# Performance work log

Measured on AMD Instinct MI355X. Metric: run time of the kernel, lower is better.

Reference implementation:

```python
import jax, jax.numpy as jnp
import numpy as np

MARGIN = 1.0  # cur_margin for LBA_inverted_loss=True
COS_SCALE = 128.0


def smoothed_metric_loss(X, margin=MARGIN):
    # X: [B, E]. Lifted structured loss with inverted cosine similarity.
    B = X.shape[0]
    P = B // 2
    D = (X @ X.T) / COS_SCALE            # [B, B]
    E = jnp.exp(margin + D)              # [B, B]
    # For pair p (rows i=2p, j=2p+1): sum E over rows {i,j}, all columns except {i,j}.
    Eb = E.reshape(P, 2, P, 2)           # [P, 2, P, 2]
    row_sums = Eb.sum(axis=(1, 2, 3))    # [P] full sum over both rows of pair p
    idx = jnp.arange(P)
    diag_block = Eb[idx, :, idx, :].sum(axis=(1, 2))  # [P] the excluded 2x2 block
    S = row_sums - diag_block            # [P] masked sums
    Dij = D.reshape(P, 2, P, 2)[idx, 0, idx, 1]       # [P] D[i, j]
    J = jnp.log(S) - Dij
    return 0.5 * jnp.mean(J * J)


def reference(text_embeddings, shape_embeddings):
    B = text_embeddings.shape[0]
    # shape_embeddings repeated twice per model: row k -> shape[k // 2]
    shape_rep = jnp.repeat(shape_embeddings, 2, axis=0)      # [B, E]
    metric_tt = smoothed_metric_loss(text_embeddings)
    # mask rows: even rows keep text, odd rows take repeated shape embedding
    even = (jnp.arange(B) % 2 == 0)[:, None]
    mixed = jnp.where(even, text_embeddings, shape_rep)      # [B, E]
    metric_st = smoothed_metric_loss(mixed)
    return metric_tt + metric_st


def setup_inputs() -> dict:
    key = jax.random.key(0)
    k1, k2 = jax.random.split(key)
    B, E = 8192, 128
    text_embeddings = jax.random.normal(k1, (B, E), dtype=jnp.float32)
    shape_embeddings = jax.random.normal(k2, (B // 2, E), dtype=jnp.float32)
    return {"text_embeddings": text_embeddings, "shape_embeddings": shape_embeddings}
```

## Files before the change

### kernel.cpp

```cpp
#include <hip/hip_runtime.h>
#include <hip/hip_bf16.h>


#define B_ROWS 8192
#define E_COLS 128
#define P_PAIRS 4096
#define NSTRIP 128
#define NHS 6

using f32x4 = __attribute__((ext_vector_type(4))) float;
using i32x8 = __attribute__((ext_vector_type(8))) int;

#define BF_SCALE 0.106164482742544f
#define EULER    2.718281828459045f
#define SCALE1   0x7f

__device__ __forceinline__ unsigned pk4_fp8(float a, float b, float c, float d) {
    unsigned v = 0;
    v = __builtin_amdgcn_cvt_pk_fp8_f32(a * BF_SCALE, b * BF_SCALE, v, false);
    v = __builtin_amdgcn_cvt_pk_fp8_f32(c * BF_SCALE, d * BF_SCALE, v, true);
    return v;
}

__device__ __forceinline__ int lds_off(int row, int k0) {
    return (row << 7) + (k0 ^ ((row & 7) << 4));
}

__device__ __forceinline__ i32x8 load_frag32(const char* base, int row, int k32) {
    union { i32x8 v; int4 h[2]; } u;
    u.h[0] = *(const int4*)(base + lds_off(row, k32));
    u.h[1] = *(const int4*)(base + lds_off(row, k32 + 16));
    return u.v;
}

__device__ __forceinline__ void stage8k(const char* gsrc, char* ldst, int tid) {
#pragma unroll
    for (int it = 0; it < 2; ++it) {
        int L   = it * 4096 + tid * 16;
        int row = L >> 7;
        int cb  = L & 127;
        int src = (row << 7) + (cb ^ ((row & 7) << 4));
        __builtin_amdgcn_global_load_lds(
            (const __attribute__((address_space(1))) void*)(gsrc + src),
            (__attribute__((address_space(3))) void*)(ldst + L), 16, 0, 0);
    }
}

__global__ void convert_kernel(const float* __restrict__ text,
                               const float* __restrict__ shape,
                               unsigned* __restrict__ Xt,
                               unsigned* __restrict__ Xm,
                               float* __restrict__ R,
                               float* __restrict__ out) {
    int idx = blockIdx.x * blockDim.x + threadIdx.x;
    if (idx >= B_ROWS * E_COLS / 4) return;
    if (idx < 4096) {
        float4 z; z.x = z.y = z.z = z.w = 0.f;
        ((float4*)R)[idx] = z;
    }
    if (idx == 0) *out = 0.f;
    int e = idx * 4;
    float4 t = *(const float4*)(text + e);
    unsigned tp = pk4_fp8(t.x, t.y, t.z, t.w);
    Xt[idx] = tp;
    int row = e >> 7;
    if (row & 1) {
        int col = e & 127;
        float4 s = *(const float4*)(shape + (row >> 1) * E_COLS + col);
        Xm[idx] = pk4_fp8(s.x, s.y, s.z, s.w);
    } else {
        Xm[idx] = tp;
    }
}

__launch_bounds__(256, 6)
__global__ void gemm_rowsum_kernel(const unsigned char* __restrict__ Xt,
                                   const unsigned char* __restrict__ Xm,
                                   float* __restrict__ R) {
    const int bm = blockIdx.x, h = blockIdx.y, l = blockIdx.z;
    const char* gX = (const char*)(l ? Xm : Xt);

    __shared__ __align__(16) char buf0[64 * 128];
    __shared__ __align__(16) char buf1[64 * 128];
    const int tid = threadIdx.x;

    const int t0 = h + 1;
    int N = (h < 3) ? 11 : 10;
    const bool do64 = (h == 4 && bm < 64);
    if (do64) N = 11;

    auto tf = [&](int i) -> int { return (h == 4 && i == 10) ? 64 : (t0 + 6 * i); };

    stage8k(gX + (size_t)bm * 8192, buf0, tid);
    stage8k(gX + (size_t)((bm + tf(0)) & 127) * 8192, buf1, tid);
    asm volatile("s_waitcnt vmcnt(2)" ::: "memory");
    __builtin_amdgcn_s_barrier();

    const int lane = tid & 63;
    const int w  = tid >> 6;
    const int wr = w >> 1, wc = w & 1;
    const int rA0 = wr * 32 + (lane & 15);
    const int rB0 = wc * 32 + (lane & 15);
    const int k32 = (lane >> 4) * 32;

    i32x8 afr[2];
#pragma unroll
    for (int m = 0; m < 2; ++m)
        afr[m] = load_frag32(buf0, rA0 + m * 16, k32);

    float s_r[2][4] = {{0.f}};

    if (h == 3) {
        i32x8 bfr[2];
#pragma unroll
        for (int n = 0; n < 2; ++n)
            bfr[n] = load_frag32(buf0, rB0 + n * 16, k32);
        f32x4 acc[2][2] = {};
#pragma unroll
        for (int m = 0; m < 2; ++m)
#pragma unroll
            for (int n = 0; n < 2; ++n)
                acc[m][n] = __builtin_amdgcn_mfma_scale_f32_16x16x128_f8f6f4(
                    afr[m], bfr[n], acc[m][n], 0, 0, 0, SCALE1, 0, SCALE1);
#pragma unroll
        for (int m = 0; m < 2; ++m)
#pragma unroll
            for (int n = 0; n < 2; ++n)
#pragma unroll
                for (int j = 0; j < 4; ++j)
                    s_r[m][j] += __builtin_amdgcn_exp2f(acc[m][n][j]);
    }

    asm volatile("s_waitcnt lgkmcnt(0)" ::: "memory");
    __builtin_amdgcn_s_barrier();

    int cur = 1;
    for (int idx = 0; idx < N; ++idx) {
        const bool hasnext = (idx + 1 < N);
        if (hasnext)
            stage8k(gX + (size_t)((bm + tf(idx + 1)) & 127) * 8192,
                    cur ? buf0 : buf1, tid);

        if (hasnext) { asm volatile("s_waitcnt vmcnt(2)" ::: "memory"); }
        else         { asm volatile("s_waitcnt vmcnt(0)" ::: "memory"); }
        __builtin_amdgcn_s_barrier();

        const char* lsrc = cur ? buf1 : buf0;
        i32x8 bfr[2];
#pragma unroll
        for (int n = 0; n < 2; ++n)
            bfr[n] = load_frag32(lsrc, rB0 + n * 16, k32);
        f32x4 acc[2][2] = {};
#pragma unroll
        for (int m = 0; m < 2; ++m)
#pragma unroll
            for (int n = 0; n < 2; ++n)
                acc[m][n] = __builtin_amdgcn_mfma_scale_f32_16x16x128_f8f6f4(
                    afr[m], bfr[n], acc[m][n], 0, 0, 0, SCALE1, 0, SCALE1);

        asm volatile("s_waitcnt lgkmcnt(0)" ::: "memory");
        __builtin_amdgcn_s_barrier();

        const int bn = (bm + tf(idx)) & 127;
        float s_c[2] = {0.f, 0.f};
#pragma unroll
        for (int m = 0; m < 2; ++m)
#pragma unroll
            for (int n = 0; n < 2; ++n)
#pragma unroll
                for (int j = 0; j < 4; ++j) {
                    float e2 = __builtin_amdgcn_exp2f(acc[m][n][j]);
                    s_r[m][j] += e2;
                    s_c[n] += e2;
                }
#pragma unroll
        for (int n = 0; n < 2; ++n) {
            float v = s_c[n];
            v += __shfl_xor(v, 16, 64);
            v += __shfl_xor(v, 32, 64);
            if (lane < 16) {
                int gcol = bn * 64 + wc * 32 + n * 16 + lane;
                atomicAdd(&R[l * B_ROWS + gcol], EULER * v);
            }
        }
        cur ^= 1;
    }

#pragma unroll
    for (int m = 0; m < 2; ++m)
#pragma unroll
        for (int j = 0; j < 4; ++j) {
            float v = s_r[m][j];
            v += __shfl_xor(v, 1, 64);
            v += __shfl_xor(v, 2, 64);
            v += __shfl_xor(v, 4, 64);
            v += __shfl_xor(v, 8, 64);
            if ((lane & 15) == 0) {
                int grow = bm * 64 + wr * 32 + m * 16 + (lane >> 4) * 4 + j;
                atomicAdd(&R[l * B_ROWS + grow], EULER * v);
            }
        }
}

__global__ void finalize_kernel(const float* __restrict__ text,
                                const float* __restrict__ shape,
                                const float* __restrict__ R,
                                float* __restrict__ out) {
    const int tid = threadIdx.x;
    const int lane = tid & 63;
    const int w = tid >> 6;
    const float inv128 = 0.0078125f;
    float accum = 0.f;

    for (int task = blockIdx.x * 4 + w; task < 2 * P_PAIRS; task += 1024) {
        int l = task >> 12;
        int p = task & (P_PAIRS - 1);
        const float* a = text + (2 * p) * E_COLS;
        const float* b = l ? (shape + p * E_COLS) : (text + (2 * p + 1) * E_COLS);
        float2 av = *(const float2*)(a + lane * 2);
        float2 bv = *(const float2*)(b + lane * 2);
        float dii = av.x * av.x + av.y * av.y;
        float djj = bv.x * bv.x + bv.y * bv.y;
        float dij = av.x * bv.x + av.y * bv.y;
#pragma unroll
        for (int sh = 1; sh < 64; sh <<= 1) {
            dii += __shfl_xor(dii, sh, 64);
            djj += __shfl_xor(djj, sh, 64);
            dij += __shfl_xor(dij, sh, 64);
        }
        if (lane == 0) {
            float Dii = dii * inv128, Djj = djj * inv128, Dij = dij * inv128;
            float S = R[l * B_ROWS + 2 * p] + R[l * B_ROWS + 2 * p + 1]
                    - (__expf(1.f + Dii) + 2.f * __expf(1.f + Dij) + __expf(1.f + Djj));
            float J = __logf(S) - Dij;
            accum += 0.5f * J * J * (1.0f / (float)P_PAIRS);
        }
    }

    __shared__ float red[4];
    if (lane == 0) red[w] = accum;
    __syncthreads();
    if (tid == 0) atomicAdd(out, red[0] + red[1] + red[2] + red[3]);
}

extern "C" void kernel_launch(void* const* d_in, const int* in_sizes, int n_in,
                              void* d_out, int out_size, void* d_ws, size_t ws_size,
                              hipStream_t stream) {
    const float* text  = (const float*)d_in[0];
    const float* shape = (const float*)d_in[1];
    float* out = (float*)d_out;
    char* ws = (char*)d_ws;

    unsigned char* Xt = (unsigned char*)ws;
    unsigned char* Xm = (unsigned char*)(ws + 1u * 1024u * 1024u);
    float* R = (float*)(ws + 2u * 1024u * 1024u);

    convert_kernel<<<(B_ROWS * E_COLS / 4 + 255) / 256, 256, 0, stream>>>(
        text, shape, (unsigned*)Xt, (unsigned*)Xm, R, out);

    dim3 grid(NSTRIP, NHS, 2);
    gemm_rowsum_kernel<<<grid, 256, 0, stream>>>(Xt, Xm, R);

    finalize_kernel<<<256, 256, 0, stream>>>(text, shape, R, out);
}
```

Before: 40.54 us.

## Remap waves to 64x16 column strips with full A-fragment residency

Each wave now holds all four A row fragments and loads a single B fragment per tile, covering a 64x16 strip instead of a 32x32 quadrant. This halves the per-tile B LDS fragment loads and column shuffle/atomic work per wave, and moves the exp2 and accumulation inside the MFMA loop with s_setprio around the MFMAs to interleave with other waves. In exchange each wave keeps more A-fragment and row-sum registers, which may pressure occupancy at launch bounds 256x6, and row-sum atomics at the end double per wave.

After: 72.62 us. 1.79x slower.

```diff
diff --git a/kernel.cpp b/kernel.cpp
--- a/kernel.cpp
+++ b/kernel.cpp
@@ -86,8 +86,7 @@
 
     const int t0 = h + 1;
     int N = (h < 3) ? 11 : 10;
-    const bool do64 = (h == 4 && bm < 64);
-    if (do64) N = 11;
+    if (h == 4 && bm < 64) N = 11;
 
     auto tf = [&](int i) -> int { return (h == 4 && i == 10) ? 64 : (t0 + 6 * i); };
 
@@ -97,38 +96,33 @@
     __builtin_amdgcn_s_barrier();
 
     const int lane = tid & 63;
-    const int w  = tid >> 6;
-    const int wr = w >> 1, wc = w & 1;
-    const int rA0 = wr * 32 + (lane & 15);
-    const int rB0 = wc * 32 + (lane & 15);
-    const int k32 = (lane >> 4) * 32;
-
-    i32x8 afr[2];
-#pragma unroll
-    for (int m = 0; m < 2; ++m)
+    const int w    = tid >> 6;
+    const int rB0  = w * 16 + (lane & 15);
+    const int rA0  = lane & 15;
+    const int k32  = (lane >> 4) * 32;
+
+    i32x8 afr[4];
+#pragma unroll
+    for (int m = 0; m < 4; ++m)
         afr[m] = load_frag32(buf0, rA0 + m * 16, k32);
 
-    float s_r[2][4] = {{0.f}};
+    float s_r[4][4] = {{0.f}};
 
     if (h == 3) {
-        i32x8 bfr[2];
-#pragma unroll
-        for (int n = 0; n < 2; ++n)
-            bfr[n] = load_frag32(buf0, rB0 + n * 16, k32);
-        f32x4 acc[2][2] = {};
-#pragma unroll
-        for (int m = 0; m < 2; ++m)
-#pragma unroll
-            for (int n = 0; n < 2; ++n)
-                acc[m][n] = __builtin_amdgcn_mfma_scale_f32_16x16x128_f8f6f4(
-                    afr[m], bfr[n], acc[m][n], 0, 0, 0, SCALE1, 0, SCALE1);
-#pragma unroll
-        for (int m = 0; m < 2; ++m)
-#pragma unroll
-            for (int n = 0; n < 2; ++n)
-#pragma unroll
-                for (int j = 0; j < 4; ++j)
-                    s_r[m][j] += __builtin_amdgcn_exp2f(acc[m][n][j]);
+        i32x8 dbf = load_frag32(buf0, rB0, k32);
+#pragma unroll
+        for (int mh = 0; mh < 2; ++mh) {
+            f32x4 a0 = {}, a1 = {};
+            a0 = __builtin_amdgcn_mfma_scale_f32_16x16x128_f8f6f4(
+                afr[2 * mh + 0], dbf, a0, 0, 0, 0, SCALE1, 0, SCALE1);
+            a1 = __builtin_amdgcn_mfma_scale_f32_16x16x128_f8f6f4(
+                afr[2 * mh + 1], dbf, a1, 0, 0, 0, SCALE1, 0, SCALE1);
+#pragma unroll
+            for (int j = 0; j < 4; ++j) {
+                s_r[2 * mh + 0][j] += __builtin_amdgcn_exp2f(a0[j]);
+                s_r[2 * mh + 1][j] += __builtin_amdgcn_exp2f(a1[j]);
+            }
+        }
     }
 
     asm volatile("s_waitcnt lgkmcnt(0)" ::: "memory");
@@ -146,48 +140,43 @@
         __builtin_amdgcn_s_barrier();
 
         const char* lsrc = cur ? buf1 : buf0;
-        i32x8 bfr[2];
-#pragma unroll
-        for (int n = 0; n < 2; ++n)
-            bfr[n] = load_frag32(lsrc, rB0 + n * 16, k32);
-        f32x4 acc[2][2] = {};
-#pragma unroll
-        for (int m = 0; m < 2; ++m)
-#pragma unroll
-            for (int n = 0; n < 2; ++n)
-                acc[m][n] = __builtin_amdgcn_mfma_scale_f32_16x16x128_f8f6f4(
-                    afr[m], bfr[n], acc[m][n], 0, 0, 0, SCALE1, 0, SCALE1);
+        i32x8 bfr = load_frag32(lsrc, rB0, k32);
+
+        float sc = 0.f;
+#pragma unroll
+        for (int mh = 0; mh < 2; ++mh) {
+            f32x4 a0 = {}, a1 = {};
+            __builtin_amdgcn_s_setprio(1);
+            a0 = __builtin_amdgcn_mfma_scale_f32_16x16x128_f8f6f4(
+                afr[2 * mh + 0], bfr, a0, 0, 0, 0, SCALE1, 0, SCALE1);
+            a1 = __builtin_amdgcn_mfma_scale_f32_16x16x128_f8f6f4(
+                afr[2 * mh + 1], bfr, a1, 0, 0, 0, SCALE1, 0, SCALE1);
+            __builtin_amdgcn_s_setprio(0);
+#pragma unroll
+            for (int j = 0; j < 4; ++j) {
+                float e0 = __builtin_amdgcn_exp2f(a0[j]);
+                float e1 = __builtin_amdgcn_exp2f(a1[j]);
+                s_r[2 * mh + 0][j] += e0;
+                s_r[2 * mh + 1][j] += e1;
+                sc += e0 + e1;
+            }
+        }
 
         asm volatile("s_waitcnt lgkmcnt(0)" ::: "memory");
         __builtin_amdgcn_s_barrier();
 
         const int bn = (bm + tf(idx)) & 127;
-        float s_c[2] = {0.f, 0.f};
-#pragma unroll
-        for (int m = 0; m < 2; ++m)
-#pragma unroll
-            for (int n = 0; n < 2; ++n)
-#pragma unroll
-                for (int j = 0; j < 4; ++j) {
-                    float e2 = __builtin_amdgcn_exp2f(acc[m][n][j]);
-                    s_r[m][j] += e2;
-                    s_c[n] += e2;
-                }
-#pragma unroll
-        for (int n = 0; n < 2; ++n) {
-            float v = s_c[n];
-            v += __shfl_xor(v, 16, 64);
-            v += __shfl_xor(v, 32, 64);
-            if (lane < 16) {
-                int gcol = bn * 64 + wc * 32 + n * 16 + lane;
-                atomicAdd(&R[l * B_ROWS + gcol], EULER * v);
-            }
+        sc += __shfl_xor(sc, 16, 64);
+        sc += __shfl_xor(sc, 32, 64);
+        if (lane < 16) {
+            int gcol = bn * 64 + w * 16 + lane;
+            atomicAdd(&R[l * B_ROWS + gcol], EULER * sc);
         }
         cur ^= 1;
     }
 
 #pragma unroll
-    for (int m = 0; m < 2; ++m)
+    for (int m = 0; m < 4; ++m)
 #pragma unroll
         for (int j = 0; j < 4; ++j) {
             float v = s_r[m][j];
@@ -196,7 +185,7 @@
             v += __shfl_xor(v, 4, 64);
             v += __shfl_xor(v, 8, 64);
             if ((lane & 15) == 0) {
-                int grow = bm * 64 + wr * 32 + m * 16 + (lane >> 4) * 4 + j;
+                int grow = bm * 64 + m * 16 + (lane >> 4) * 4 + j;
                 atomicAdd(&R[l * B_ROWS + grow], EULER * v);
             }
         }
```
